# Performance work log

Measured on AMD Instinct MI355X. Metric: run time of the kernel, lower is better.

## Reference

```python
import jax, jax.numpy as jnp
from jax import lax
import numpy as np

B, CTX, TGT, D_MODEL = 2, 1024, 256, 512
EXPAND, D_STATE, D_CONV, N_LAYERS = 2, 16, 4, 2
D_INNER = EXPAND * D_MODEL
DT_RANK = (D_MODEL + 15) // 16  # 32, mamba_ssm default ceil(d_model/16)
LN_EPS = 1e-5


def setup_inputs() -> dict:
    key = jax.random.key(0)
    ks = jax.random.split(key, 20)
    s = 0.02
    inp = {
        "context_repr": jax.random.normal(ks[0], (B, CTX, D_MODEL), jnp.float32),
        "target_time_emb": jax.random.normal(ks[1], (B, TGT, D_MODEL), jnp.float32),
        "target_var_emb": jax.random.normal(ks[2], (B, TGT, D_MODEL), jnp.float32),
        "target_count": TGT,
        # position_proj / output_proj / LayerNorm params
        "pos_w": jax.random.normal(ks[3], (D_MODEL, 2 * D_MODEL), jnp.float32) * s,
        "pos_b": jnp.zeros((D_MODEL,), jnp.float32),
        "outp_w": jax.random.normal(ks[4], (D_MODEL, D_MODEL), jnp.float32) * s,
        "outp_b": jnp.zeros((D_MODEL,), jnp.float32),
        "ln_g": jnp.ones((D_MODEL,), jnp.float32),
        "ln_b": jnp.zeros((D_MODEL,), jnp.float32),
        # stacked per-layer Mamba params
        "in_w": jax.random.normal(ks[5], (N_LAYERS, 2 * D_INNER, D_MODEL), jnp.float32) * s,
        "conv_w": jax.random.normal(ks[6], (N_LAYERS, D_INNER, D_CONV), jnp.float32) * s,
        "conv_b": jnp.zeros((N_LAYERS, D_INNER), jnp.float32),
        "xproj_w": jax.random.normal(ks[7], (N_LAYERS, DT_RANK + 2 * D_STATE, D_INNER), jnp.float32) * s,
        "dt_w": jax.random.normal(ks[8], (N_LAYERS, D_INNER, DT_RANK), jnp.float32) * s,
        "dt_b": jax.random.normal(ks[9], (N_LAYERS, D_INNER), jnp.float32) * s,
        # A_log init as in mamba_ssm: A = arange(1, d_state+1) repeated over d_inner
        "A_log": jnp.broadcast_to(
            jnp.log(jnp.arange(1, D_STATE + 1, dtype=jnp.float32)),
            (N_LAYERS, D_INNER, D_STATE),
        ).copy(),
        "D_skip": jnp.ones((N_LAYERS, D_INNER), jnp.float32),
        "out_w": jax.random.normal(ks[10], (N_LAYERS, D_MODEL, D_INNER), jnp.float32) * s,
    }
    return inp


def _mamba_block(x, in_w, conv_w, conv_b, xproj_w, dt_w, dt_b, A_log, D_skip, out_w):
    # x: [B, L, d_model]
    Bb, L, _ = x.shape
    xz = jnp.einsum("bld,ed->ble", x, in_w)          # [B, L, 2*d_inner]
    xc, z = jnp.split(xz, 2, axis=-1)
    # causal depthwise conv1d (Conv1d pad=d_conv-1 then [..., :L])
    xt = xc.transpose(0, 2, 1)                        # [B, d_inner, L]
    conv = lax.conv_general_dilated(
        xt, conv_w[:, None, :], (1,), [(D_CONV - 1, 0)],
        feature_group_count=D_INNER,
        dimension_numbers=("NCH", "OIH", "NCH"),
    )
    u = jax.nn.silu(conv + conv_b[None, :, None]).transpose(0, 2, 1)  # [B, L, d_inner]
    x_dbl = jnp.einsum("bld,ed->ble", u, xproj_w)     # [B, L, dt_rank + 2*d_state]
    dt, Bm, Cm = jnp.split(x_dbl, [DT_RANK, DT_RANK + D_STATE], axis=-1)
    delta = jax.nn.softplus(jnp.einsum("blr,dr->bld", dt, dt_w) + dt_b)  # [B, L, d_inner]
    A = -jnp.exp(A_log)                               # [d_inner, d_state]
    dA = jnp.exp(delta[..., None] * A)                # [B, L, d_inner, d_state]
    dBu = delta[..., None] * Bm[:, :, None, :] * u[..., None]

    def step(h, inps):
        dA_t, dBu_t, C_t = inps                       # [B,d_inner,d_state], same, [B,d_state]
        h = dA_t * h + dBu_t
        y = jnp.einsum("bds,bs->bd", h, C_t)
        return h, y

    h0 = jnp.zeros((Bb, D_INNER, D_STATE), x.dtype)
    _, ys = lax.scan(step, h0, (dA.transpose(1, 0, 2, 3), dBu.transpose(1, 0, 2, 3), Cm.transpose(1, 0, 2)))
    y = ys.transpose(1, 0, 2) + u * D_skip            # [B, L, d_inner]
    y = y * jax.nn.silu(z)
    return jnp.einsum("ble,de->bld", y, out_w)        # [B, L, d_model]


def reference(context_repr, target_time_emb, target_var_emb, target_count,
              pos_w, pos_b, outp_w, outp_b, ln_g, ln_b,
              in_w, conv_w, conv_b, xproj_w, dt_w, dt_b, A_log, D_skip, out_w):
    tc = jnp.concatenate([target_time_emb, target_var_emb], axis=-1)      # [B, T, 2*d]
    pos = jnp.einsum("blk,dk->bld", tc, pos_w) + pos_b                    # [B, T, d]
    x = jnp.concatenate([context_repr, pos], axis=1)                      # [B, C+T, d]
    for i in range(N_LAYERS):
        x = x + _mamba_block(x, in_w[i], conv_w[i], conv_b[i], xproj_w[i],
                             dt_w[i], dt_b[i], A_log[i], D_skip[i], out_w[i])
    mu = jnp.mean(x, axis=-1, keepdims=True)
    var = jnp.mean(jnp.square(x - mu), axis=-1, keepdims=True)
    x = (x - mu) * lax.rsqrt(var + LN_EPS) * ln_g + ln_b
    tgt = x[:, -int(target_count):]
    return jnp.einsum("bld,ed->ble", tgt, outp_w) + outp_b
```

## Files before the change

### kernel.cpp

```cpp
#include <hip/hip_runtime.h>
#include <hip/hip_bf16.h>

#define B_     2
#define CTX_   1024
#define TGT_   256
#define DM_    512
#define L_     1280
#define DI_    1024
#define DS_    16
#define DCONV_ 4
#define NL_    2
#define DTR_   32
#define MROWS_ (B_*L_)
#define NC_    80
#define CL_    16
#define XDBL_N_ (MROWS_*64)

typedef unsigned short u16;
typedef __attribute__((ext_vector_type(8))) __bf16 bf16x8;
typedef __attribute__((ext_vector_type(4))) float f32x4;

__device__ __forceinline__ float sigmoidf_(float v){ return 1.f/(1.f+__expf(-v)); }
__device__ __forceinline__ float siluf_(float v){ return v*sigmoidf_(v); }
__device__ __forceinline__ float softplusf_(float v){ return (v>20.f)?v:log1pf(__expf(v)); }
__device__ __forceinline__ u16 f2b(float f){
    union { float f; unsigned u; } x; x.f = f;
    unsigned u = x.u;
    return (u16)((u + 0x7fffu + ((u>>16)&1u)) >> 16);
}
__device__ __forceinline__ float b2f(u16 v){ return __uint_as_float(((unsigned)v)<<16); }
__device__ __forceinline__ void gload_lds16(const void* g, void* l){
    __builtin_amdgcn_global_load_lds((const __attribute__((address_space(1))) unsigned*)g,
                                     (__attribute__((address_space(3))) unsigned*)l, 16, 0, 0);
}
#define PIPE_SYNC do{ asm volatile("s_waitcnt vmcnt(0)" ::: "memory"); \
                      __builtin_amdgcn_sched_barrier(0); \
                      __builtin_amdgcn_s_barrier(); \
                      __builtin_amdgcn_sched_barrier(0); }while(0)

#define G0_ 262144
#define G1_ 131072
#define G2_  65536
#define G3_  32768
#define G4_  16384
__global__ __launch_bounds__(256) void k_init(const float* __restrict__ s0, const float* __restrict__ s1,
                                              const float* __restrict__ s2, const float* __restrict__ s3,
                                              const float* __restrict__ s4,
                                              u16* d0, u16* d1, u16* d2, u16* d3, u16* d4,
                                              const float* __restrict__ ctx, const float* __restrict__ te,
                                              const float* __restrict__ ve, float* __restrict__ x,
                                              u16* __restrict__ xb, u16* __restrict__ tcb){
    int blk = blockIdx.x;
    if (blk < 1984){
        int g = blk*256 + threadIdx.x;
        const float* s; u16* d; int base;
        if      (g < G0_)                { s=s0; d=d0; base=g*8; }
        else if (g < G0_+G1_)            { s=s1; d=d1; base=(g-G0_)*8; }
        else if (g < G0_+G1_+G2_)        { s=s2; d=d2; base=(g-G0_-G1_)*8; }
        else if (g < G0_+G1_+G2_+G3_)    { s=s3; d=d3; base=(g-G0_-G1_-G2_)*8; }
        else                             { s=s4; d=d4; base=(g-G0_-G1_-G2_-G3_)*8; }
        float4 a = *(const float4*)&s[base];
        float4 b = *(const float4*)&s[base+4];
        union { u16 us[8]; uint4 v; } o;
        o.us[0]=f2b(a.x); o.us[1]=f2b(a.y); o.us[2]=f2b(a.z); o.us[3]=f2b(a.w);
        o.us[4]=f2b(b.x); o.us[5]=f2b(b.y); o.us[6]=f2b(b.z); o.us[7]=f2b(b.w);
        *(uint4*)&d[base] = o.v;
    } else if (blk < 1984+1024){
        int e = ((blk-1984)*256 + threadIdx.x)*4;
        int d = e % DM_;
        int l = (e/DM_) % CTX_;
        int b = e/(DM_*CTX_);
        float4 v = *(const float4*)&ctx[e];
        size_t o = ((size_t)(b*L_+l))*DM_ + d;
        *(float4*)&x[o] = v;
        union { u16 us[4]; uint2 q; } p;
        p.us[0]=f2b(v.x); p.us[1]=f2b(v.y); p.us[2]=f2b(v.z); p.us[3]=f2b(v.w);
        *(uint2*)&xb[o] = p.q;
    } else {
        int e = ((blk-1984-1024)*256 + threadIdx.x)*4;
        int k = e % (2*DM_);
        int r = e / (2*DM_);
        float4 v = (k < DM_) ? *(const float4*)&te[(size_t)r*DM_ + k]
                             : *(const float4*)&ve[(size_t)r*DM_ + (k-DM_)];
        union { u16 us[4]; uint2 q; } p;
        p.us[0]=f2b(v.x); p.us[1]=f2b(v.y); p.us[2]=f2b(v.z); p.us[3]=f2b(v.w);
        *(uint2*)&tcb[e] = p.q;
    }
}

__global__ __launch_bounds__(256) void k_conv_silu(const u16* __restrict__ xzb, const float* __restrict__ cw,
                                                   const float* __restrict__ cb, u16* __restrict__ ub){
    int e = (blockIdx.x*256 + threadIdx.x)*4;
    int d = e % DI_;
    int l = (e/DI_) % L_;
    int b = e/(DI_*L_);
    const u16* base = xzb + (size_t)b*L_*2048 + d;
    float4 w0 = *(const float4*)&cw[(d+0)*4];
    float4 w1 = *(const float4*)&cw[(d+1)*4];
    float4 w2 = *(const float4*)&cw[(d+2)*4];
    float4 w3 = *(const float4*)&cw[(d+3)*4];
    float4 bb = *(const float4*)&cb[d];
    float a0=bb.x, a1=bb.y, a2=bb.z, a3=bb.w;
    #pragma unroll
    for (int k=0;k<DCONV_;++k){
        int ll = l-3+k;
        if (ll >= 0){
            uint2 q = *(const uint2*)&base[(size_t)ll*2048];
            float x0=b2f((u16)(q.x&0xffffu)), x1=b2f((u16)(q.x>>16));
            float x2=b2f((u16)(q.y&0xffffu)), x3=b2f((u16)(q.y>>16));
            float c0 = (k==0)?w0.x:(k==1)?w0.y:(k==2)?w0.z:w0.w;
            float c1 = (k==0)?w1.x:(k==1)?w1.y:(k==2)?w1.z:w1.w;
            float c2 = (k==0)?w2.x:(k==1)?w2.y:(k==2)?w2.z:w2.w;
            float c3 = (k==0)?w3.x:(k==1)?w3.y:(k==2)?w3.z:w3.w;
            a0=fmaf(x0,c0,a0); a1=fmaf(x1,c1,a1); a2=fmaf(x2,c2,a2); a3=fmaf(x3,c3,a3);
        }
    }
    union { u16 us[4]; uint2 q; } o;
    o.us[0]=f2b(siluf_(a0)); o.us[1]=f2b(siluf_(a1));
    o.us[2]=f2b(siluf_(a2)); o.us[3]=f2b(siluf_(a3));
    *(uint2*)&ub[e] = o.q;
}

template<bool WB>
__global__ __launch_bounds__(512) void k_mmx(const u16* __restrict__ A, int lda,
                                             const u16* __restrict__ Bw, int ldb,
                                             float* __restrict__ C, int ldc,
                                             const float* __restrict__ bias, int K,
                                             u16* __restrict__ Cb, int ldcb){
    __shared__ u16 As[2][128*32];
    __shared__ u16 Bs[2][128*32];
    int tid = threadIdx.x;
    int wave = tid >> 6, lane = tid & 63;
    int bm = blockIdx.y*128, bn = blockIdx.x*128;
    int wr = (wave>>2)*64, wc = (wave&3)*32;
    f32x4 acc[4][2] = {};
    int lrow = lane & 15, lk = (lane>>4)*8;
    int dphys = tid*16;
    int alog  = dphys ^ (((dphys>>7)&7)<<4);
    int grow  = alog >> 6;
    int gcol  = (alog & 63) >> 1;
    const u16* Ar = A  + (size_t)(bm+grow)*lda + gcol;
    const u16* Br = Bw + (size_t)(bn+grow)*ldb + gcol;
    int aoff[4], boff[2];
    #pragma unroll
    for (int f=0; f<4; ++f){
        int ra = wr + f*16 + lrow;
        aoff[f] = (ra*64 + lk*2) ^ (((ra>>1)&7)<<4);
    }
    #pragma unroll
    for (int f=0; f<2; ++f){
        int rb = wc + f*16 + lrow;
        boff[f] = (rb*64 + lk*2) ^ (((rb>>1)&7)<<4);
    }
    int nt = K >> 5;
    auto stage = [&](int t, int buf){
        int k0 = t*32;
        gload_lds16(Ar + k0, &As[buf][wave*512]);
        gload_lds16(Br + k0, &Bs[buf][wave*512]);
    };
    stage(0, 0);
    PIPE_SYNC;
    int cur = 0;
    for (int t=0; t<nt; ++t){
        if (t+1 < nt) stage(t+1, cur^1);
        bf16x8 af[4], bfr[2];
        #pragma unroll
        for (int f=0; f<4; ++f) af[f]  = *(const bf16x8*)((const char*)As[cur] + aoff[f]);
        #pragma unroll
        for (int f=0; f<2; ++f) bfr[f] = *(const bf16x8*)((const char*)Bs[cur] + boff[f]);
        #pragma unroll
        for (int fm=0; fm<4; ++fm)
            #pragma unroll
            for (int fn=0; fn<2; ++fn)
                acc[fm][fn] = __builtin_amdgcn_mfma_f32_16x16x32_bf16(af[fm], bfr[fn], acc[fm][fn], 0,0,0);
        PIPE_SYNC;
        cur ^= 1;
    }
    #pragma unroll
    for (int fm=0; fm<4; ++fm){
        int m0 = bm + wr + fm*16 + (lane>>4)*4;
        #pragma unroll
        for (int fn=0; fn<2; ++fn){
            int n = bn + wc + fn*16 + (lane&15);
            float bsv = (!WB && bias) ? bias[n] : 0.f;
            #pragma unroll
            for (int j=0; j<4; ++j){
                float v = acc[fm][fn][j] + bsv;
                if (WB) Cb[(size_t)(m0+j)*ldcb + n] = f2b(v);
                else    C [(size_t)(m0+j)*ldc  + n] = v;
            }
        }
    }
}

template<bool ACC, bool SPLIT, bool SCAT>
__global__ __launch_bounds__(512) void k_mmx64(const u16* __restrict__ A, int lda,
                                               const u16* __restrict__ Bw, int ldb,
                                               float* __restrict__ C, int ldc,
                                               const float* __restrict__ bias, int ksteps,
                                               u16* __restrict__ Cb, int ldcb, int splitStride){
    __shared__ u16 As[2][64*32];
    __shared__ u16 Bs[2][64*32];
    int tid = threadIdx.x;
    int wave = tid >> 6, lane = tid & 63;
    int bm = blockIdx.y*64;
    int bn    = SPLIT ? 0 : blockIdx.x*64;
    int kbase = SPLIT ? blockIdx.x*ksteps*32 : 0;
    int wr = (wave>>2)*32, wc = (wave&3)*16;
    f32x4 acc[2] = {};
    int lrow = lane & 15, lk = (lane>>4)*8;
    int w4 = wave & 3;
    int dphys = w4*1024 + lane*16;
    int alog  = dphys ^ (((dphys>>7)&7)<<4);
    int grow  = alog >> 6;
    int gcol  = (alog & 63) >> 1;
    bool isB = wave >= 4;
    const u16* Sr = isB ? (Bw + (size_t)(bn+grow)*ldb + gcol)
                        : (A  + (size_t)(bm+grow)*lda + gcol);
    u16* dst0 = isB ? &Bs[0][w4*512] : &As[0][w4*512];
    u16* dst1 = isB ? &Bs[1][w4*512] : &As[1][w4*512];
    int aoff[2], boff;
    #pragma unroll
    for (int f=0; f<2; ++f){
        int ra = wr + f*16 + lrow;
        aoff[f] = (ra*64 + lk*2) ^ (((ra>>1)&7)<<4);
    }
    { int rb = wc + lrow; boff = (rb*64 + lk*2) ^ (((rb>>1)&7)<<4); }
    auto stage = [&](int t, int buf){
        gload_lds16(Sr + kbase + t*32, buf ? dst1 : dst0);
    };
    stage(0, 0);
    PIPE_SYNC;
    int cur = 0;
    for (int t = 0; t < ksteps; ++t){
        if (t+1 < ksteps) stage(t+1, cur^1);
        bf16x8 af[2], bfr;
        #pragma unroll
        for (int f=0; f<2; ++f) af[f] = *(const bf16x8*)((const char*)As[cur] + aoff[f]);
        bfr = *(const bf16x8*)((const char*)Bs[cur] + boff);
        #pragma unroll
        for (int fm=0; fm<2; ++fm)
            acc[fm] = __builtin_amdgcn_mfma_f32_16x16x32_bf16(af[fm], bfr, acc[fm], 0,0,0);
        PIPE_SYNC;
        cur ^= 1;
    }
    float* Cout = SPLIT ? (C + (size_t)blockIdx.x*splitStride) : C;
    #pragma unroll
    for (int fm=0; fm<2; ++fm){
        int m0 = bm + wr + fm*16 + (lane>>4)*4;
        int n = bn + wc + (lane&15);
        float bsv = (!SPLIT && bias) ? bias[n] : 0.f;
        #pragma unroll
        for (int j=0; j<4; ++j){
            float v = acc[fm][j] + bsv;
            int m = m0 + j;
            if (SCAT){
                int xrow = (m>>8)*L_ + CTX_ + (m&255);
                C [(size_t)xrow*ldc  + n] = v;
                Cb[(size_t)xrow*ldcb + n] = f2b(v);
            } else {
                size_t off = (size_t)m*ldc + n;
                if (ACC) v += Cout[off];
                Cout[off] = v;
                if (!SPLIT && Cb) Cb[(size_t)m*ldcb + n] = f2b(v);
            }
        }
    }
}

__global__ __launch_bounds__(256) void k_scan1(const u16* __restrict__ ub, const float* __restrict__ xdblp,
                                               const float* __restrict__ dtw, const float* __restrict__ dtb,
                                               const float* __restrict__ Alog,
                                               float* __restrict__ hend, float* __restrict__ P){
    __shared__ float sX[CL_*64];
    __shared__ float sW[64*33];
    __shared__ float sDtb[64];
    __shared__ float sDel[CL_*64];
    __shared__ u16   sU[CL_*64];
    int blk = blockIdx.x;
    int dgrp = blk & 15;
    int c = (blk>>4) % NC_;
    int b = blk/(16*NC_);
    int d0 = dgrp*64;
    int tid = threadIdx.x;
    size_t rowbase = (size_t)(b*L_ + c*CL_);
    {
        int e = tid*4;
        float4 s4 = *(const float4*)&xdblp[rowbase*64 + e];
        #pragma unroll
        for (int p=1;p<8;++p){
            float4 t4 = *(const float4*)&xdblp[(size_t)p*XDBL_N_ + rowbase*64 + e];
            s4.x+=t4.x; s4.y+=t4.y; s4.z+=t4.z; s4.w+=t4.w;
        }
        *(float4*)&sX[e] = s4;
        int st=e>>6, dd=e&63;
        *(uint2*)&sU[e] = *(const uint2*)&ub[(rowbase+st)*DI_ + d0 + dd];
        int w0 = tid*8, dr = w0>>5, kk = w0&31;
        float4 wa = *(const float4*)&dtw[(size_t)(d0+dr)*DTR_ + kk];
        float4 wb = *(const float4*)&dtw[(size_t)(d0+dr)*DTR_ + kk + 4];
        sW[dr*33+kk+0]=wa.x; sW[dr*33+kk+1]=wa.y; sW[dr*33+kk+2]=wa.z; sW[dr*33+kk+3]=wa.w;
        sW[dr*33+kk+4]=wb.x; sW[dr*33+kk+5]=wb.y; sW[dr*33+kk+6]=wb.z; sW[dr*33+kk+7]=wb.w;
        if (tid < 64) sDtb[tid] = dtb[d0+tid];
    }
    __syncthreads();
    #pragma unroll
    for (int i=0;i<4;++i){
        int idx = tid + i*256;
        int t = idx>>6, dd = idx&63;
        float acc = sDtb[dd];
        #pragma unroll
        for (int k=0;k<DTR_;++k) acc = fmaf(sX[t*64+k], sW[dd*33+k], acc);
        sDel[idx] = softplusf_(acc);
    }
    __syncthreads();
    int dl = tid>>2, sg = (tid&3)*4;
    int d = d0 + dl;
    float A[4];
    #pragma unroll
    for (int i=0;i<4;++i) A[i] = -__expf(Alog[d*DS_ + sg + i]);
    float h[4] = {0,0,0,0}, Pl[4] = {1.f,1.f,1.f,1.f};
    #pragma unroll
    for (int t=0;t<CL_;++t){
        float delta = sDel[t*64+dl];
        float uu    = b2f(sU[t*64+dl]);
        float du    = delta*uu;
        #pragma unroll
        for (int i=0;i<4;++i){
            float a = __expf(delta*A[i]);
            h[i]  = fmaf(a, h[i], du*sX[t*64 + 32 + sg + i]);
            Pl[i] *= a;
        }
    }
    size_t ob = ((size_t)((b*NC_+c)*DI_) + d)*DS_ + sg;
    *(float4*)&hend[ob] = make_float4(h[0],h[1],h[2],h[3]);
    *(float4*)&P[ob]    = make_float4(Pl[0],Pl[1],Pl[2],Pl[3]);
}

__global__ __launch_bounds__(256) void k_scan2(float* __restrict__ hend, const float* __restrict__ P){
    int g = blockIdx.x*256 + threadIdx.x;
    int s = g & 15;
    int d = (g>>4) & 1023;
    int b = g>>14;
    size_t base = ((size_t)b*NC_*DI_ + d)*DS_ + s;
    const size_t cs = (size_t)DI_*DS_;
    float h = 0.f;
    for (int c0=0;c0<NC_;c0+=8){
        float he[8], p[8];
        #pragma unroll
        for (int j=0;j<8;++j){ size_t idx = base + (size_t)(c0+j)*cs; he[j]=hend[idx]; p[j]=P[idx]; }
        #pragma unroll
        for (int j=0;j<8;++j){ size_t idx = base + (size_t)(c0+j)*cs; hend[idx]=h; h=fmaf(p[j],h,he[j]); }
    }
}

__global__ __launch_bounds__(256) void k_scan3(const u16* __restrict__ ub, const float* __restrict__ xdblp,
                                               const float* __restrict__ dtw, const float* __restrict__ dtb,
                                               const u16* __restrict__ xzb,
                                               const float* __restrict__ Alog, const float* __restrict__ Dsk,
                                               const float* __restrict__ hstart, u16* __restrict__ yb){
    __shared__ float sX[CL_*64];
    __shared__ float sW[64*33];
    __shared__ float sDtb[64];
    __shared__ float sDel[CL_*64];
    __shared__ u16   sU[CL_*64];
    __shared__ float sY[CL_*64];
    int blk = blockIdx.x;
    int dgrp = blk & 15;
    int c = (blk>>4) % NC_;
    int b = blk/(16*NC_);
    int d0 = dgrp*64;
    int tid = threadIdx.x;
    size_t rowbase = (size_t)(b*L_ + c*CL_);
    {
        int e = tid*4;
        float4 s4 = *(const float4*)&xdblp[rowbase*64 + e];
        #pragma unroll
        for (int p=1;p<8;++p){
            float4 t4 = *(const float4*)&xdblp[(size_t)p*XDBL_N_ + rowbase*64 + e];
            s4.x+=t4.x; s4.y+=t4.y; s4.z+=t4.z; s4.w+=t4.w;
        }
        *(float4*)&sX[e] = s4;
        int st=e>>6, dd=e&63;
        *(uint2*)&sU[e] = *(const uint2*)&ub[(rowbase+st)*DI_ + d0 + dd];
        int w0 = tid*8, dr = w0>>5, kk = w0&31;
        float4 wa = *(const float4*)&dtw[(size_t)(d0+dr)*DTR_ + kk];
        float4 wb = *(const float4*)&dtw[(size_t)(d0+dr)*DTR_ + kk + 4];
        sW[dr*33+kk+0]=wa.x; sW[dr*33+kk+1]=wa.y; sW[dr*33+kk+2]=wa.z; sW[dr*33+kk+3]=wa.w;
        sW[dr*33+kk+4]=wb.x; sW[dr*33+kk+5]=wb.y; sW[dr*33+kk+6]=wb.z; sW[dr*33+kk+7]=wb.w;
        if (tid < 64) sDtb[tid] = dtb[d0+tid];
    }
    __syncthreads();
    #pragma unroll
    for (int i=0;i<4;++i){
        int idx = tid + i*256;
        int t = idx>>6, dd = idx&63;
        float acc = sDtb[dd];
        #pragma unroll
        for (int k=0;k<DTR_;++k) acc = fmaf(sX[t*64+k], sW[dd*33+k], acc);
        sDel[idx] = softplusf_(acc);
    }
    __syncthreads();
    int dl = tid>>2, sg = (tid&3)*4;
    int d = d0 + dl;
    float A[4];
    #pragma unroll
    for (int i=0;i<4;++i) A[i] = -__expf(Alog[d*DS_ + sg + i]);
    size_t ib = ((size_t)((b*NC_+c)*DI_) + d)*DS_ + sg;
    float4 h4 = *(const float4*)&hstart[ib];
    float h[4] = {h4.x, h4.y, h4.z, h4.w};
    #pragma unroll
    for (int t=0;t<CL_;++t){
        float delta = sDel[t*64+dl];
        float uu    = b2f(sU[t*64+dl]);
        float du    = delta*uu;
        float yt = 0.f;
        #pragma unroll
        for (int i=0;i<4;++i){
            float a = __expf(delta*A[i]);
            h[i] = fmaf(a, h[i], du*sX[t*64 + 32 + sg + i]);
            yt   = fmaf(h[i], sX[t*64 + 48 + sg + i], yt);
        }
        yt += __shfl_xor(yt, 1);
        yt += __shfl_xor(yt, 2);
        if ((tid&3)==0) sY[t*64+dl] = yt;
    }
    __syncthreads();
    {
        int e = tid*4, st = e>>6, dd = e&63;
        size_t off = (rowbase+st)*DI_ + d0 + dd;
        float4 dskv = *(const float4*)&Dsk[d0+dd];
        uint2 zz = *(const uint2*)&xzb[(rowbase+st)*2048 + DI_ + d0 + dd];
        float z0 = __uint_as_float(zz.x<<16),  z1 = __uint_as_float(zz.x & 0xffff0000u);
        float z2 = __uint_as_float(zz.y<<16),  z3 = __uint_as_float(zz.y & 0xffff0000u);
        float u0 = b2f(sU[e+0]), u1 = b2f(sU[e+1]), u2 = b2f(sU[e+2]), u3 = b2f(sU[e+3]);
        union { u16 us[4]; uint2 q; } o;
        o.us[0] = f2b((sY[e+0] + u0*dskv.x) * siluf_(z0));
        o.us[1] = f2b((sY[e+1] + u1*dskv.y) * siluf_(z1));
        o.us[2] = f2b((sY[e+2] + u2*dskv.z) * siluf_(z2));
        o.us[3] = f2b((sY[e+3] + u3*dskv.w) * siluf_(z3));
        *(uint2*)&yb[off] = o.q;
    }
}

__global__ __launch_bounds__(256) void k_ln_tgt(const float* __restrict__ x, const float* __restrict__ g_,
                                                const float* __restrict__ b_, u16* __restrict__ xnb){
    int r = blockIdx.x;
    int b = r / TGT_, t = r % TGT_;
    const float* row = x + ((size_t)(b*L_+CTX_+t))*DM_;
    int tid = threadIdx.x;
    float2 v = *(const float2*)&row[tid*2];
    float s = v.x+v.y, sq = v.x*v.x+v.y*v.y;
    #pragma unroll
    for (int off=32; off; off>>=1){ s += __shfl_down(s,off); sq += __shfl_down(sq,off); }
    __shared__ float ss[4], ssq[4];
    int w = tid>>6, ln = tid&63;
    if (ln==0){ ss[w]=s; ssq[w]=sq; }
    __syncthreads();
    if (tid==0){
        float S=ss[0]+ss[1]+ss[2]+ss[3], Q=ssq[0]+ssq[1]+ssq[2]+ssq[3];
        float mu = S/(float)DM_;
        float var = Q/(float)DM_ - mu*mu;
        ss[0]=mu; ssq[0]=rsqrtf(var+1e-5f);
    }
    __syncthreads();
    float mu=ss[0], rs=ssq[0];
    xnb[(size_t)r*DM_ + tid*2+0] = f2b((v.x-mu)*rs*g_[tid*2+0] + b_[tid*2+0]);
    xnb[(size_t)r*DM_ + tid*2+1] = f2b((v.y-mu)*rs*g_[tid*2+1] + b_[tid*2+1]);
}

extern "C" void kernel_launch(void* const* d_in, const int* in_sizes, int n_in,
                              void* d_out, int out_size, void* d_ws, size_t ws_size,
                              hipStream_t stream) {
    const float* ctx    = (const float*)d_in[0];
    const float* te     = (const float*)d_in[1];
    const float* ve     = (const float*)d_in[2];
    const float* pos_w  = (const float*)d_in[4];
    const float* pos_b  = (const float*)d_in[5];
    const float* outp_w = (const float*)d_in[6];
    const float* outp_b = (const float*)d_in[7];
    const float* ln_g   = (const float*)d_in[8];
    const float* ln_b   = (const float*)d_in[9];
    const float* in_w   = (const float*)d_in[10];
    const float* conv_w = (const float*)d_in[11];
    const float* conv_b = (const float*)d_in[12];
    const float* xproj_w= (const float*)d_in[13];
    const float* dt_w   = (const float*)d_in[14];
    const float* dt_b   = (const float*)d_in[15];
    const float* A_log  = (const float*)d_in[16];
    const float* D_skip = (const float*)d_in[17];
    const float* out_w  = (const float*)d_in[18];
    float* out = (float*)d_out;

    float* ws    = (float*)d_ws;
    float* x     = ws;
    float* hend  = x     + 1310720;
    float* P     = hend  + 2621440;
    float* xdblp = P     + 2621440;
    u16*  xb    = (u16*)(xdblp + 1310720);
    u16*  tcb   = xb    + 1310720;
    u16*  yb    = tcb   + 524288;
    u16*  xnb   = yb    + 2621440;
    u16*  ub    = xnb   + 262144;
    u16*  xzb   = ub    + 2621440;
    u16*  inwb  = xzb   + 5242880;
    u16*  outwb = inwb  + 2097152;
    u16*  poswb = outwb + 1048576;
    u16*  outpwb= poswb + 524288;
    u16*  xpwb  = outpwb+ 262144;

    k_init<<<3520, 256, 0, stream>>>(in_w, out_w, pos_w, outp_w, xproj_w,
                                     inwb, outwb, poswb, outpwb, xpwb,
                                     ctx, te, ve, x, xb, tcb);
    k_mmx64<false,false,true><<<dim3(8,8), 512, 0, stream>>>(tcb, 2*DM_, poswb, 2*DM_, x, DM_, pos_b, 32, xb, DM_, 0);

    for (int i=0;i<NL_;++i){
        const u16*   inwbi  = inwb + (size_t)i*2*DI_*DM_;
        const float* cw     = conv_w  + (size_t)i*DI_*DCONV_;
        const float* cb     = conv_b  + (size_t)i*DI_;
        const u16*   xpwbi  = xpwb + (size_t)i*(DTR_+2*DS_)*DI_;
        const float* dtw    = dt_w    + (size_t)i*DI_*DTR_;
        const float* dtb    = dt_b    + (size_t)i*DI_;
        const float* Ai     = A_log   + (size_t)i*DI_*DS_;
        const float* Dsk    = D_skip  + (size_t)i*DI_;
        const u16*   outwbi = outwb + (size_t)i*DM_*DI_;

        k_mmx<true><<<dim3(16,20), 512, 0, stream>>>(xb, DM_, inwbi, DM_, nullptr, 0, nullptr, DM_, xzb, 2*DI_);
        k_conv_silu<<<2560, 256, 0, stream>>>(xzb, cw, cb, ub);
        k_mmx64<false,true,false><<<dim3(8,40), 512, 0, stream>>>(ub, DI_, xpwbi, DI_, xdblp, 64, nullptr, 4, nullptr, 0, XDBL_N_);
        k_scan1<<<2560, 256, 0, stream>>>(ub, xdblp, dtw, dtb, Ai, hend, P);
        k_scan2<<<128, 256, 0, stream>>>(hend, P);
        k_scan3<<<2560, 256, 0, stream>>>(ub, xdblp, dtw, dtb, xzb, Ai, Dsk, hend, yb);
        k_mmx64<true,false,false><<<dim3(8,40), 512, 0, stream>>>(yb, DI_, outwbi, DI_, x, DM_, nullptr, 32, xb, DM_, 0);
    }

    k_ln_tgt<<<512, 256, 0, stream>>>(x, ln_g, ln_b, xnb);
    k_mmx64<false,false,false><<<dim3(8,8), 512, 0, stream>>>(xnb, DM_, outpwb, DM_, out, DM_, outp_b, 16, nullptr, 0, 0);
}
```

Baseline: 238.2 us.

## Fuse causal conv+SiLU into x_proj and scan kernels; deepen in_proj K tile

Removes the standalone conv+SiLU kernel and its bf16 u buffer. The depthwise causal conv and SiLU are now recomputed from xzb inside the x_proj split-K GEMM, k_scan1 and k_scan3, with u kept in fp32 in shared memory. The in_proj GEMM now stages 64-wide K tiles (two k-substeps per sync), which halves barrier count but doubles LDS use. The trade is redundant conv recomputation in three kernels and a non-double-buffered x_proj loop with extra syncs, in exchange for one fewer launch and no u round trip through memory.

Result: slower. 244.0 us (+2.4%).

```diff
diff --git a/kernel.cpp b/kernel.cpp
--- a/kernel.cpp
+++ b/kernel.cpp
@@ -88,91 +88,69 @@
     }
 }
 
-__global__ __launch_bounds__(256) void k_conv_silu(const u16* __restrict__ xzb, const float* __restrict__ cw,
-                                                   const float* __restrict__ cb, u16* __restrict__ ub){
-    int e = (blockIdx.x*256 + threadIdx.x)*4;
-    int d = e % DI_;
-    int l = (e/DI_) % L_;
-    int b = e/(DI_*L_);
-    const u16* base = xzb + (size_t)b*L_*2048 + d;
-    float4 w0 = *(const float4*)&cw[(d+0)*4];
-    float4 w1 = *(const float4*)&cw[(d+1)*4];
-    float4 w2 = *(const float4*)&cw[(d+2)*4];
-    float4 w3 = *(const float4*)&cw[(d+3)*4];
-    float4 bb = *(const float4*)&cb[d];
-    float a0=bb.x, a1=bb.y, a2=bb.z, a3=bb.w;
-    #pragma unroll
-    for (int k=0;k<DCONV_;++k){
-        int ll = l-3+k;
-        if (ll >= 0){
-            uint2 q = *(const uint2*)&base[(size_t)ll*2048];
-            float x0=b2f((u16)(q.x&0xffffu)), x1=b2f((u16)(q.x>>16));
-            float x2=b2f((u16)(q.y&0xffffu)), x3=b2f((u16)(q.y>>16));
-            float c0 = (k==0)?w0.x:(k==1)?w0.y:(k==2)?w0.z:w0.w;
-            float c1 = (k==0)?w1.x:(k==1)?w1.y:(k==2)?w1.z:w1.w;
-            float c2 = (k==0)?w2.x:(k==1)?w2.y:(k==2)?w2.z:w2.w;
-            float c3 = (k==0)?w3.x:(k==1)?w3.y:(k==2)?w3.z:w3.w;
-            a0=fmaf(x0,c0,a0); a1=fmaf(x1,c1,a1); a2=fmaf(x2,c2,a2); a3=fmaf(x3,c3,a3);
-        }
-    }
-    union { u16 us[4]; uint2 q; } o;
-    o.us[0]=f2b(siluf_(a0)); o.us[1]=f2b(siluf_(a1));
-    o.us[2]=f2b(siluf_(a2)); o.us[3]=f2b(siluf_(a3));
-    *(uint2*)&ub[e] = o.q;
-}
-
 template<bool WB>
 __global__ __launch_bounds__(512) void k_mmx(const u16* __restrict__ A, int lda,
                                              const u16* __restrict__ Bw, int ldb,
                                              float* __restrict__ C, int ldc,
                                              const float* __restrict__ bias, int K,
                                              u16* __restrict__ Cb, int ldcb){
-    __shared__ u16 As[2][128*32];
-    __shared__ u16 Bs[2][128*32];
+    __shared__ u16 As[2][128*64];
+    __shared__ u16 Bs[2][128*64];
     int tid = threadIdx.x;
     int wave = tid >> 6, lane = tid & 63;
     int bm = blockIdx.y*128, bn = blockIdx.x*128;
     int wr = (wave>>2)*64, wc = (wave&3)*32;
     f32x4 acc[4][2] = {};
     int lrow = lane & 15, lk = (lane>>4)*8;
-    int dphys = tid*16;
-    int alog  = dphys ^ (((dphys>>7)&7)<<4);
-    int grow  = alog >> 6;
-    int gcol  = (alog & 63) >> 1;
-    const u16* Ar = A  + (size_t)(bm+grow)*lda + gcol;
-    const u16* Br = Bw + (size_t)(bn+grow)*ldb + gcol;
-    int aoff[4], boff[2];
+    int dphys0 = tid*16;
+    int dphys1 = dphys0 + 8192;
+    int alog0  = dphys0 ^ (((dphys0>>7)&7)<<4);
+    int alog1  = dphys1 ^ (((dphys1>>7)&7)<<4);
+    int grow0  = alog0 >> 7,         grow1 = alog1 >> 7;
+    int gcol0  = (alog0 & 127) >> 1, gcol1 = (alog1 & 127) >> 1;
+    const u16* Ar0 = A  + (size_t)(bm+grow0)*lda + gcol0;
+    const u16* Ar1 = A  + (size_t)(bm+grow1)*lda + gcol1;
+    const u16* Br0 = Bw + (size_t)(bn+grow0)*ldb + gcol0;
+    const u16* Br1 = Bw + (size_t)(bn+grow1)*ldb + gcol1;
+    int aoff[4][2], boff[2][2];
     #pragma unroll
     for (int f=0; f<4; ++f){
         int ra = wr + f*16 + lrow;
-        aoff[f] = (ra*64 + lk*2) ^ (((ra>>1)&7)<<4);
+        #pragma unroll
+        for (int s=0;s<2;++s) aoff[f][s] = (ra*128 + s*64 + lk*2) ^ ((ra&7)<<4);
     }
     #pragma unroll
     for (int f=0; f<2; ++f){
         int rb = wc + f*16 + lrow;
-        boff[f] = (rb*64 + lk*2) ^ (((rb>>1)&7)<<4);
-    }
-    int nt = K >> 5;
+        #pragma unroll
+        for (int s=0;s<2;++s) boff[f][s] = (rb*128 + s*64 + lk*2) ^ ((rb&7)<<4);
+    }
+    int nt = K >> 6;
     auto stage = [&](int t, int buf){
-        int k0 = t*32;
-        gload_lds16(Ar + k0, &As[buf][wave*512]);
-        gload_lds16(Br + k0, &Bs[buf][wave*512]);
+        int k0 = t*64;
+        gload_lds16(Ar0 + k0, &As[buf][wave*512]);
+        gload_lds16(Ar1 + k0, &As[buf][4096 + wave*512]);
+        gload_lds16(Br0 + k0, &Bs[buf][wave*512]);
+        gload_lds16(Br1 + k0, &Bs[buf][4096 + wave*512]);
     };
     stage(0, 0);
     PIPE_SYNC;
     int cur = 0;
     for (int t=0; t<nt; ++t){
         if (t+1 < nt) stage(t+1, cur^1);
-        bf16x8 af[4], bfr[2];
-        #pragma unroll
-        for (int f=0; f<4; ++f) af[f]  = *(const bf16x8*)((const char*)As[cur] + aoff[f]);
-        #pragma unroll
-        for (int f=0; f<2; ++f) bfr[f] = *(const bf16x8*)((const char*)Bs[cur] + boff[f]);
-        #pragma unroll
-        for (int fm=0; fm<4; ++fm)
+        #pragma unroll
+        for (int s=0;s<2;++s){
+            bf16x8 af[4], bfr[2];
             #pragma unroll
-            for (int fn=0; fn<2; ++fn)
-                acc[fm][fn] = __builtin_amdgcn_mfma_f32_16x16x32_bf16(af[fm], bfr[fn], acc[fm][fn], 0,0,0);
+            for (int f=0; f<4; ++f) af[f]  = *(const bf16x8*)((const char*)As[cur] + aoff[f][s]);
+            #pragma unroll
+            for (int f=0; f<2; ++f) bfr[f] = *(const bf16x8*)((const char*)Bs[cur] + boff[f][s]);
+            #pragma unroll
+            for (int fm=0; fm<4; ++fm)
+                #pragma unroll
+                for (int fn=0; fn<2; ++fn)
+                    acc[fm][fn] = __builtin_amdgcn_mfma_f32_16x16x32_bf16(af[fm], bfr[fn], acc[fm][fn], 0,0,0);
+        }
         PIPE_SYNC;
         cur ^= 1;
     }
@@ -193,19 +171,18 @@
     }
 }
 
-template<bool ACC, bool SPLIT, bool SCAT>
+template<bool ACC, bool SCAT>
 __global__ __launch_bounds__(512) void k_mmx64(const u16* __restrict__ A, int lda,
                                                const u16* __restrict__ Bw, int ldb,
                                                float* __restrict__ C, int ldc,
                                                const float* __restrict__ bias, int ksteps,
-                                               u16* __restrict__ Cb, int ldcb, int splitStride){
+                                               u16* __restrict__ Cb, int ldcb){
     __shared__ u16 As[2][64*32];
     __shared__ u16 Bs[2][64*32];
     int tid = threadIdx.x;
     int wave = tid >> 6, lane = tid & 63;
     int bm = blockIdx.y*64;
-    int bn    = SPLIT ? 0 : blockIdx.x*64;
-    int kbase = SPLIT ? blockIdx.x*ksteps*32 : 0;
+    int bn = blockIdx.x*64;
     int wr = (wave>>2)*32, wc = (wave&3)*16;
     f32x4 acc[2] = {};
     int lrow = lane & 15, lk = (lane>>4)*8;
@@ -227,7 +204,7 @@
     }
     { int rb = wc + lrow; boff = (rb*64 + lk*2) ^ (((rb>>1)&7)<<4); }
     auto stage = [&](int t, int buf){
-        gload_lds16(Sr + kbase + t*32, buf ? dst1 : dst0);
+        gload_lds16(Sr + t*32, buf ? dst1 : dst0);
     };
     stage(0, 0);
     PIPE_SYNC;
@@ -244,12 +221,11 @@
         PIPE_SYNC;
         cur ^= 1;
     }
-    float* Cout = SPLIT ? (C + (size_t)blockIdx.x*splitStride) : C;
     #pragma unroll
     for (int fm=0; fm<2; ++fm){
         int m0 = bm + wr + fm*16 + (lane>>4)*4;
         int n = bn + wc + (lane&15);
-        float bsv = (!SPLIT && bias) ? bias[n] : 0.f;
+        float bsv = bias ? bias[n] : 0.f;
         #pragma unroll
         for (int j=0; j<4; ++j){
             float v = acc[fm][j] + bsv;
@@ -260,23 +236,100 @@
                 Cb[(size_t)xrow*ldcb + n] = f2b(v);
             } else {
                 size_t off = (size_t)m*ldc + n;
-                if (ACC) v += Cout[off];
-                Cout[off] = v;
-                if (!SPLIT && Cb) Cb[(size_t)m*ldcb + n] = f2b(v);
+                if (ACC) v += C[off];
+                C[off] = v;
+                if (Cb) Cb[(size_t)m*ldcb + n] = f2b(v);
             }
         }
     }
 }
 
-__global__ __launch_bounds__(256) void k_scan1(const u16* __restrict__ ub, const float* __restrict__ xdblp,
+__global__ __launch_bounds__(512) void k_xproj(const u16* __restrict__ xzb, const u16* __restrict__ Bw,
+                                               float* __restrict__ C, const float* __restrict__ cw,
+                                               const float* __restrict__ cb){
+    __shared__ u16 As[64*32];
+    __shared__ u16 Bs[64*32];
+    __shared__ u16 sXC[67*32];
+    int tid = threadIdx.x;
+    int wave = tid >> 6, lane = tid & 63;
+    int bm = blockIdx.y*64;
+    int kbase = blockIdx.x*128;
+    int b0row = (bm/L_)*L_;
+    int wr = (wave>>2)*32, wc = (wave&3)*16;
+    f32x4 acc[2] = {};
+    int lrow = lane & 15, lk = (lane>>4)*8;
+    int w4 = wave & 3;
+    int dphys = w4*1024 + lane*16;
+    int alog  = dphys ^ (((dphys>>7)&7)<<4);
+    int grow  = alog >> 6;
+    int gcol  = (alog & 63) >> 1;
+    const u16* Br = Bw + (size_t)grow*DI_ + gcol;
+    int aoff[2], boff;
+    #pragma unroll
+    for (int f=0; f<2; ++f){
+        int ra = wr + f*16 + lrow;
+        aoff[f] = (ra*64 + lk*2) ^ (((ra>>1)&7)<<4);
+    }
+    { int rb = wc + lrow; boff = (rb*64 + lk*2) ^ (((rb>>1)&7)<<4); }
+    for (int t = 0; t < 4; ++t){
+        int k0 = kbase + t*32;
+        if (wave >= 4) gload_lds16(Br + k0, &Bs[w4*512]);
+        for (int i = tid; i < 67*32; i += 512){
+            int rr = i >> 5, cc = i & 31;
+            int gr = bm + rr - 3;
+            sXC[i] = (gr >= b0row) ? xzb[(size_t)gr*2048 + k0 + cc] : (u16)0;
+        }
+        __syncthreads();
+        {
+            int o = tid*4, rr = o >> 5, cc0 = o & 31;
+            union { u16 us[4]; uint2 q; } w;
+            #pragma unroll
+            for (int j=0;j<4;++j){
+                int cc = cc0 + j, d = k0 + cc;
+                float4 wv = *(const float4*)&cw[d*4];
+                float a = cb[d];
+                a = fmaf(b2f(sXC[(rr+0)*32+cc]), wv.x, a);
+                a = fmaf(b2f(sXC[(rr+1)*32+cc]), wv.y, a);
+                a = fmaf(b2f(sXC[(rr+2)*32+cc]), wv.z, a);
+                a = fmaf(b2f(sXC[(rr+3)*32+cc]), wv.w, a);
+                w.us[j] = f2b(siluf_(a));
+            }
+            int L0 = rr*64 + cc0*2;
+            int ph = L0 ^ (((L0>>7)&7)<<4);
+            *(uint2*)((char*)As + ph) = w.q;
+        }
+        __syncthreads();
+        bf16x8 af[2], bfr;
+        #pragma unroll
+        for (int f=0; f<2; ++f) af[f] = *(const bf16x8*)((const char*)As + aoff[f]);
+        bfr = *(const bf16x8*)((const char*)Bs + boff);
+        #pragma unroll
+        for (int fm=0; fm<2; ++fm)
+            acc[fm] = __builtin_amdgcn_mfma_f32_16x16x32_bf16(af[fm], bfr, acc[fm], 0,0,0);
+        __syncthreads();
+    }
+    float* Cout = C + (size_t)blockIdx.x*XDBL_N_;
+    #pragma unroll
+    for (int fm=0; fm<2; ++fm){
+        int m0 = bm + wr + fm*16 + (lane>>4)*4;
+        int n = wc + (lane&15);
+        #pragma unroll
+        for (int j=0; j<4; ++j)
+            Cout[(size_t)(m0+j)*64 + n] = acc[fm][j];
+    }
+}
+
+__global__ __launch_bounds__(256) void k_scan1(const u16* __restrict__ xzb, const float* __restrict__ xdblp,
                                                const float* __restrict__ dtw, const float* __restrict__ dtb,
+                                               const float* __restrict__ cw, const float* __restrict__ cb,
                                                const float* __restrict__ Alog,
                                                float* __restrict__ hend, float* __restrict__ P){
     __shared__ float sX[CL_*64];
     __shared__ float sW[64*33];
     __shared__ float sDtb[64];
     __shared__ float sDel[CL_*64];
-    __shared__ u16   sU[CL_*64];
+    __shared__ float sU[CL_*64];
+    __shared__ u16   sXC[19*64];
     int blk = blockIdx.x;
     int dgrp = blk & 15;
     int c = (blk>>4) % NC_;
@@ -293,8 +346,6 @@
             s4.x+=t4.x; s4.y+=t4.y; s4.z+=t4.z; s4.w+=t4.w;
         }
         *(float4*)&sX[e] = s4;
-        int st=e>>6, dd=e&63;
-        *(uint2*)&sU[e] = *(const uint2*)&ub[(rowbase+st)*DI_ + d0 + dd];
         int w0 = tid*8, dr = w0>>5, kk = w0&31;
         float4 wa = *(const float4*)&dtw[(size_t)(d0+dr)*DTR_ + kk];
         float4 wb = *(const float4*)&dtw[(size_t)(d0+dr)*DTR_ + kk + 4];
@@ -302,7 +353,26 @@
         sW[dr*33+kk+4]=wb.x; sW[dr*33+kk+5]=wb.y; sW[dr*33+kk+6]=wb.z; sW[dr*33+kk+7]=wb.w;
         if (tid < 64) sDtb[tid] = dtb[d0+tid];
     }
+    for (int i = tid; i < 19*64; i += 256){
+        int rr = i >> 6, dd = i & 63;
+        long gr = (long)rowbase + rr - 3;
+        sXC[i] = (gr >= (long)b*L_) ? xzb[(size_t)gr*2048 + d0 + dd] : (u16)0;
+    }
     __syncthreads();
+    {
+        int o = tid*4, t = o>>6, dd0 = o&63;
+        #pragma unroll
+        for (int j=0;j<4;++j){
+            int dd = dd0 + j, d = d0 + dd;
+            float4 wv = *(const float4*)&cw[d*4];
+            float a = cb[d];
+            a = fmaf(b2f(sXC[(t+0)*64+dd]), wv.x, a);
+            a = fmaf(b2f(sXC[(t+1)*64+dd]), wv.y, a);
+            a = fmaf(b2f(sXC[(t+2)*64+dd]), wv.z, a);
+            a = fmaf(b2f(sXC[(t+3)*64+dd]), wv.w, a);
+            sU[t*64+dd] = siluf_(a);
+        }
+    }
     #pragma unroll
     for (int i=0;i<4;++i){
         int idx = tid + i*256;
@@ -322,8 +392,7 @@
     #pragma unroll
     for (int t=0;t<CL_;++t){
         float delta = sDel[t*64+dl];
-        float uu    = b2f(sU[t*64+dl]);
-        float du    = delta*uu;
+        float du    = delta*sU[t*64+dl];
         #pragma unroll
         for (int i=0;i<4;++i){
             float a = __expf(delta*A[i]);
@@ -353,17 +422,18 @@
     }
 }
 
-__global__ __launch_bounds__(256) void k_scan3(const u16* __restrict__ ub, const float* __restrict__ xdblp,
+__global__ __launch_bounds__(256) void k_scan3(const u16* __restrict__ xzb, const float* __restrict__ xdblp,
                                                const float* __restrict__ dtw, const float* __restrict__ dtb,
-                                               const u16* __restrict__ xzb,
+                                               const float* __restrict__ cw, const float* __restrict__ cb,
                                                const float* __restrict__ Alog, const float* __restrict__ Dsk,
                                                const float* __restrict__ hstart, u16* __restrict__ yb){
     __shared__ float sX[CL_*64];
     __shared__ float sW[64*33];
     __shared__ float sDtb[64];
     __shared__ float sDel[CL_*64];
-    __shared__ u16   sU[CL_*64];
+    __shared__ float sU[CL_*64];
     __shared__ float sY[CL_*64];
+    __shared__ u16   sXC[19*64];
     int blk = blockIdx.x;
     int dgrp = blk & 15;
     int c = (blk>>4) % NC_;
@@ -380,8 +450,6 @@
             s4.x+=t4.x; s4.y+=t4.y; s4.z+=t4.z; s4.w+=t4.w;
         }
         *(float4*)&sX[e] = s4;
-        int st=e>>6, dd=e&63;
-        *(uint2*)&sU[e] = *(const uint2*)&ub[(rowbase+st)*DI_ + d0 + dd];
         int w0 = tid*8, dr = w0>>5, kk = w0&31;
         float4 wa = *(const float4*)&dtw[(size_t)(d0+dr)*DTR_ + kk];
         float4 wb = *(const float4*)&dtw[(size_t)(d0+dr)*DTR_ + kk + 4];
@@ -389,7 +457,26 @@
         sW[dr*33+kk+4]=wb.x; sW[dr*33+kk+5]=wb.y; sW[dr*33+kk+6]=wb.z; sW[dr*33+kk+7]=wb.w;
         if (tid < 64) sDtb[tid] = dtb[d0+tid];
     }
+    for (int i = tid; i < 19*64; i += 256){
+        int rr = i >> 6, dd = i & 63;
+        long gr = (long)rowbase + rr - 3;
+        sXC[i] = (gr >= (long)b*L_) ? xzb[(size_t)gr*2048 + d0 + dd] : (u16)0;
+    }
     __syncthreads();
+    {
+        int o = tid*4, t = o>>6, dd0 = o&63;
+        #pragma unroll
+        for (int j=0;j<4;++j){
+            int dd = dd0 + j, d = d0 + dd;
+            float4 wv = *(const float4*)&cw[d*4];
+            float a = cb[d];
+            a = fmaf(b2f(sXC[(t+0)*64+dd]), wv.x, a);
+            a = fmaf(b2f(sXC[(t+1)*64+dd]), wv.y, a);
+            a = fmaf(b2f(sXC[(t+2)*64+dd]), wv.z, a);
+            a = fmaf(b2f(sXC[(t+3)*64+dd]), wv.w, a);
+            sU[t*64+dd] = siluf_(a);
+        }
+    }
     #pragma unroll
     for (int i=0;i<4;++i){
         int idx = tid + i*256;
@@ -411,8 +498,7 @@
     #pragma unroll
     for (int t=0;t<CL_;++t){
         float delta = sDel[t*64+dl];
-        float uu    = b2f(sU[t*64+dl]);
-        float du    = delta*uu;
+        float du    = delta*sU[t*64+dl];
         float yt = 0.f;
         #pragma unroll
         for (int i=0;i<4;++i){
@@ -432,12 +518,11 @@
         uint2 zz = *(const uint2*)&xzb[(rowbase+st)*2048 + DI_ + d0 + dd];
         float z0 = __uint_as_float(zz.x<<16),  z1 = __uint_as_float(zz.x & 0xffff0000u);
         float z2 = __uint_as_float(zz.y<<16),  z3 = __uint_as_float(zz.y & 0xffff0000u);
-        float u0 = b2f(sU[e+0]), u1 = b2f(sU[e+1]), u2 = b2f(sU[e+2]), u3 = b2f(sU[e+3]);
         union { u16 us[4]; uint2 q; } o;
-        o.us[0] = f2b((sY[e+0] + u0*dskv.x) * siluf_(z0));
-        o.us[1] = f2b((sY[e+1] + u1*dskv.y) * siluf_(z1));
-        o.us[2] = f2b((sY[e+2] + u2*dskv.z) * siluf_(z2));
-        o.us[3] = f2b((sY[e+3] + u3*dskv.w) * siluf_(z3));
+        o.us[0] = f2b((sY[e+0] + sU[e+0]*dskv.x) * siluf_(z0));
+        o.us[1] = f2b((sY[e+1] + sU[e+1]*dskv.y) * siluf_(z1));
+        o.us[2] = f2b((sY[e+2] + sU[e+2]*dskv.z) * siluf_(z2));
+        o.us[3] = f2b((sY[e+3] + sU[e+3]*dskv.w) * siluf_(z3));
         *(uint2*)&yb[off] = o.q;
     }
 }
@@ -500,8 +585,7 @@
     u16*  tcb   = xb    + 1310720;
     u16*  yb    = tcb   + 524288;
     u16*  xnb   = yb    + 2621440;
-    u16*  ub    = xnb   + 262144;
-    u16*  xzb   = ub    + 2621440;
+    u16*  xzb   = xnb   + 262144;
     u16*  inwb  = xzb   + 5242880;
     u16*  outwb = inwb  + 2097152;
     u16*  poswb = outwb + 1048576;
@@ -511,7 +595,7 @@
     k_init<<<3520, 256, 0, stream>>>(in_w, out_w, pos_w, outp_w, xproj_w,
                                      inwb, outwb, poswb, outpwb, xpwb,
                                      ctx, te, ve, x, xb, tcb);
-    k_mmx64<false,false,true><<<dim3(8,8), 512, 0, stream>>>(tcb, 2*DM_, poswb, 2*DM_, x, DM_, pos_b, 32, xb, DM_, 0);
+    k_mmx64<false,true><<<dim3(8,8), 512, 0, stream>>>(tcb, 2*DM_, poswb, 2*DM_, x, DM_, pos_b, 32, xb, DM_);
 
     for (int i=0;i<NL_;++i){
         const u16*   inwbi  = inwb + (size_t)i*2*DI_*DM_;
@@ -525,14 +609,13 @@
         const u16*   outwbi = outwb + (size_t)i*DM_*DI_;
 
         k_mmx<true><<<dim3(16,20), 512, 0, stream>>>(xb, DM_, inwbi, DM_, nullptr, 0, nullptr, DM_, xzb, 2*DI_);
-        k_conv_silu<<<2560, 256, 0, stream>>>(xzb, cw, cb, ub);
-        k_mmx64<false,true,false><<<dim3(8,40), 512, 0, stream>>>(ub, DI_, xpwbi, DI_, xdblp, 64, nullptr, 4, nullptr, 0, XDBL_N_);
-        k_scan1<<<2560, 256, 0, stream>>>(ub, xdblp, dtw, dtb, Ai, hend, P);
+        k_xproj<<<dim3(8,40), 512, 0, stream>>>(xzb, xpwbi, xdblp, cw, cb);
+        k_scan1<<<2560, 256, 0, stream>>>(xzb, xdblp, dtw, dtb, cw, cb, Ai, hend, P);
         k_scan2<<<128, 256, 0, stream>>>(hend, P);
-        k_scan3<<<2560, 256, 0, stream>>>(ub, xdblp, dtw, dtb, xzb, Ai, Dsk, hend, yb);
-        k_mmx64<true,false,false><<<dim3(8,40), 512, 0, stream>>>(yb, DI_, outwbi, DI_, x, DM_, nullptr, 32, xb, DM_, 0);
+        k_scan3<<<2560, 256, 0, stream>>>(xzb, xdblp, dtw, dtb, cw, cb, Ai, Dsk, hend, yb);
+        k_mmx64<true,false><<<dim3(8,40), 512, 0, stream>>>(yb, DI_, outwbi, DI_, x, DM_, nullptr, 32, xb, DM_);
     }
 
     k_ln_tgt<<<512, 256, 0, stream>>>(x, ln_g, ln_b, xnb);
-    k_mmx64<false,false,false><<<dim3(8,8), 512, 0, stream>>>(xnb, DM_, outpwb, DM_, out, DM_, outp_b, 16, nullptr, 0, 0);
-}
+    k_mmx64<false,false><<<dim3(8,8), 512, 0, stream>>>(xnb, DM_, outpwb, DM_, out, DM_, outp_b, 16, nullptr, 0);
+}
```
